# Performance work log

Hardware: AMD Instinct MI355X
Metric: run time of the kernel (lower is better)

Reference implementation:

```python
import jax, jax.numpy as jnp
import numpy as np

N_SPECIES = 119
N_RADIAL = 5
N_BASIS = 7
R_MIN = 0.5
R_MAX = 6.0
UNITS = (512, 512)
EMB_NORM = 1.0 / np.sqrt(N_BASIS)
N_ATOMS = 20000
N_PAIRS = 800000
N_FEAT = 360  # gaussian moments for n_radial=5, n_contr=8

# triangular index sets for symmetric contractions
_t2i, _t2j = np.tril_indices(N_RADIAL)  # 15 unique (r,s) pairs
_t3 = np.array([(i, j, k) for i in range(N_RADIAL) for j in range(i + 1) for k in range(j + 1)])
_t3i, _t3j, _t3k = _t3[:, 0], _t3[:, 1], _t3[:, 2]  # 35 unique (r,s,t) triples


def _forward(R, Z, neighbor, offsets, embeddings, W1, b1, W2, b2, W3, b3):
    n_atoms = R.shape[0]
    idx_i, idx_j = neighbor[0], neighbor[1]
    # --- distance computation (free space, init_box == 0) ---
    dr_vec = R[idx_j] - R[idx_i] + offsets                      # (P,3)
    dr = jnp.sqrt(jnp.sum(dr_vec * dr_vec, axis=-1))            # (P,)
    dn = dr_vec / (dr + 1e-5)[:, None]                          # unit vectors
    # --- gaussian radial basis + species-pair embedding + cosine cutoff ---
    shifts = jnp.linspace(R_MIN, R_MAX, N_BASIS)
    betta = N_BASIS ** 2 / R_MAX ** 2
    rad_norm = (2.0 * betta / np.pi) ** 0.75
    basis = rad_norm * jnp.exp(-betta * (dr[:, None] - shifts) ** 2)   # (P,B)
    cutoff = 0.5 * (jnp.cos(np.pi * dr / R_MAX) + 1.0) * (dr < R_MAX)
    emb = embeddings[Z[idx_j], Z[idx_i]]                               # (P,R,B)
    radial = EMB_NORM * jnp.einsum('prb,pb->pr', emb, basis) * cutoff[:, None]  # (P,R)
    # --- geometric moments, aggregated per central atom ---
    m1 = radial[:, :, None] * dn[:, None, :]                    # (P,R,3)
    m2 = m1[..., None] * dn[:, None, None, :]                   # (P,R,3,3)
    m3 = m2[..., None] * dn[:, None, None, None, :]             # (P,R,3,3,3)
    seg = lambda x: jax.ops.segment_sum(x, idx_i, num_segments=n_atoms)
    M0, M1, M2, M3 = seg(radial), seg(m1), seg(m2), seg(m3)
    # --- invariant contractions (gaussian moments) ---
    c1 = jnp.einsum('ari,asi->ars', M1, M1)[:, _t2i, _t2j]
    c2 = jnp.einsum('arij,asij->ars', M2, M2)[:, _t2i, _t2j]
    c3 = jnp.einsum('arijk,asijk->ars', M3, M3)[:, _t2i, _t2j]
    c4 = jnp.einsum('arij,asik,atjk->arst', M2, M2, M2)[:, _t3i, _t3j, _t3k]
    c5 = jnp.einsum('ari,asj,atij->arst', M1, M1, M2)[:, _t2i, _t2j].reshape(n_atoms, -1)
    c6 = jnp.einsum('arijk,asijl,atkl->arst', M3, M3, M2)[:, _t2i, _t2j].reshape(n_atoms, -1)
    c7 = jnp.einsum('arijk,asij,atk->arst', M3, M2, M1).reshape(n_atoms, -1)
    feats = jnp.concatenate([M0, c1, c2, c3, c4, c5, c6, c7], axis=-1)  # (A,360)
    # --- vmapped per-atom NTK readout MLP (swish) ---
    h = jax.nn.swish(feats @ W1 / np.sqrt(N_FEAT) + 0.1 * b1)
    h = jax.nn.swish(h @ W2 / np.sqrt(UNITS[0]) + 0.1 * b2)
    out = h @ W3 / np.sqrt(UNITS[1]) + 0.1 * b3                 # (A,1)
    # --- mask padded atoms (Z == 0) ---
    out = out * (Z > 0)[:, None]
    return out


def setup_inputs() -> dict:
    key = jax.random.key(0)
    ks = jax.random.split(key, 8)
    R = jax.random.uniform(ks[0], (N_ATOMS, 3), jnp.float32) * 12.0  # 12 A cube
    Z = jax.random.randint(ks[1], (N_ATOMS,), 0, N_SPECIES, jnp.int32)
    neighbor = jax.random.randint(ks[2], (2, N_PAIRS), 0, N_ATOMS, jnp.int32)
    # avoid degenerate self pairs (dr == 0 would NaN the unit vector grad)
    idx_i, idx_j = neighbor[0], neighbor[1]
    idx_j = jnp.where(idx_j == idx_i, (idx_j + 1) % N_ATOMS, idx_j)
    neighbor = jnp.stack([idx_i, idx_j], axis=0)
    box = jnp.zeros((3, 3), jnp.float32)
    offsets = jnp.zeros((N_PAIRS, 3), jnp.float32)
    embeddings = jax.random.normal(ks[3], (N_SPECIES, N_SPECIES, N_RADIAL, N_BASIS), jnp.float32)
    W1 = jax.random.normal(ks[4], (N_FEAT, UNITS[0]), jnp.float32)
    b1 = jnp.zeros((UNITS[0],), jnp.float32)
    W2 = jax.random.normal(ks[5], (UNITS[0], UNITS[1]), jnp.float32)
    b2 = jnp.zeros((UNITS[1],), jnp.float32)
    W3 = jax.random.normal(ks[6], (UNITS[1], 1), jnp.float32)
    b3 = jnp.zeros((1,), jnp.float32)
    return dict(R=R, Z=Z, neighbor=neighbor, box=box, offsets=offsets,
                embeddings=embeddings, W1=W1, b1=b1, W2=W2, b2=b2, W3=W3, b3=b3)


def reference(R, Z, neighbor, box, offsets, embeddings, W1, b1, W2, b2, W3, b3):
    # box is unused: init_box == 0 selects the free-space displacement fn
    return _forward(R, Z, neighbor, offsets, embeddings, W1, b1, W2, b2, W3, b3)
```

## Files before the change

### kernel.cpp

```cpp
#include <hip/hip_runtime.h>
#include <hip/hip_bf16.h>
#include <cmath>

#define NSP 119
#define UNITS 512
#define NFEAT 360
#define KP1 384
#define CAP 128

typedef __attribute__((ext_vector_type(8))) short short8;
typedef __attribute__((ext_vector_type(4))) float floatx4;

__device__ __host__ constexpr int s2c(int i, int j) {
    return (i > j) ? i*(i+1)/2 + j : j*(j+1)/2 + i;
}
__device__ __host__ constexpr int s3c(int x, int y, int z) {
    int A = x > y ? x : y; A = A > z ? A : z;
    int C = x < y ? x : y; C = C < z ? C : z;
    int B = x + y + z - A - C;
    return A*(A+1)*(A+2)/6 + B*(B+1)/2 + C;
}

struct BasisConsts {
    float f0k;
    float kg;
    float scale;
    float c[6];
};

__global__ __launch_bounds__(256) void prep_kernel(
    const float* __restrict__ W1, const float* __restrict__ W2,
    __hip_bfloat16* __restrict__ W1t, __hip_bfloat16* __restrict__ W2t,
    int* __restrict__ counts, float* __restrict__ outbuf,
    const int* __restrict__ Z, const float* __restrict__ b3, int natoms)
{
    int b = blockIdx.x;
    if (b < 448) {
        __shared__ float tile[32][33];
        const float* W; __hip_bfloat16* Wt; int K, Kp, ik, in;
        if (b < 192) { W = W1; Wt = W1t; K = NFEAT; Kp = KP1; ik = b % 12; in = b / 12; }
        else { int b2 = b - 192; W = W2; Wt = W2t; K = UNITS; Kp = UNITS; ik = b2 & 15; in = b2 >> 4; }
        int tx = threadIdx.x & 31, ty = threadIdx.x >> 5;
        int n = in * 32 + tx;
        #pragma unroll
        for (int pp = 0; pp < 4; ++pp) {
            int kk = ty + pp * 8;
            int k = ik * 32 + kk;
            tile[kk][tx] = (k < K) ? W[(size_t)k * UNITS + n] : 0.f;
        }
        __syncthreads();
        #pragma unroll
        for (int pp = 0; pp < 4; ++pp) {
            int nn = ty + pp * 8;
            Wt[(size_t)(in * 32 + nn) * Kp + ik * 32 + tx] = __float2bfloat16(tile[tx][nn]);
        }
    } else {
        int idx = (b - 448) * 256 + threadIdx.x;
        if (idx < natoms) {
            counts[idx] = 0;
            outbuf[idx] = (Z[idx] > 0) ? 0.1f * b3[0] : 0.f;
        }
    }
}

__global__ __launch_bounds__(256) void pair_compute_kernel(
    const float* __restrict__ R, const int* __restrict__ Z,
    const int* __restrict__ nbr, const float* __restrict__ offsets,
    const float* __restrict__ emb, int* __restrict__ counts,
    float* __restrict__ tmpRec, int npairs, BasisConsts bc)
{
    int p = blockIdx.x * 256 + threadIdx.x;
    if (p >= npairs) return;
    int i = nbr[p];
    int j = nbr[npairs + p];
    float dx = R[3*j]   - R[3*i]   + offsets[3*p];
    float dy = R[3*j+1] - R[3*i+1] + offsets[3*p+1];
    float dz = R[3*j+2] - R[3*i+2] + offsets[3*p+2];
    float dr2 = fmaf(dz, dz, fmaf(dy, dy, dx*dx));
    if (dr2 >= 36.0f) return;
    int pos = atomicAdd(&counts[i], 1);
    if (pos >= CAP) return;

    float dr  = sqrtf(dr2);
    float inv = 1.0f / (dr + 1e-5f);
    float d0  = dr - 0.5f;
    float basis[7];
    basis[0] = exp2f(bc.f0k * d0 * d0);
    float G  = exp2f(bc.kg * dr);
    float cur = basis[0];
    #pragma unroll
    for (int b = 0; b < 6; ++b) { cur *= G * bc.c[b]; basis[b+1] = cur; }
    float cut = 0.5f * (__cosf(dr * 0.52359877559829887f) + 1.0f);
    float s = bc.scale * cut;

    const float* e = emb + ((size_t)Z[j] * NSP + Z[i]) * 35;
    float ev[35];
    __builtin_memcpy(ev, e, 35 * sizeof(float));

    float rec[8];
    #pragma unroll
    for (int r = 0; r < 5; ++r) {
        float acc = 0.f;
        #pragma unroll
        for (int b = 0; b < 7; ++b) acc += ev[r*7+b] * basis[b];
        rec[r] = s * acc;
    }
    rec[5] = dx * inv; rec[6] = dy * inv; rec[7] = dz * inv;
    float4* out = (float4*)(tmpRec + ((size_t)i * CAP + pos) * 8);
    out[0] = make_float4(rec[0], rec[1], rec[2], rec[3]);
    out[1] = make_float4(rec[4], rec[5], rec[6], rec[7]);
}

#define SREC 28
__global__ __launch_bounds__(256) void moment_kernel(
    const float* __restrict__ tmpRec, const int* __restrict__ counts,
    float* __restrict__ momG, int natoms)
{
    int wv = threadIdx.x >> 6, lane = threadIdx.x & 63;
    int a = blockIdx.x * 4 + wv;
    __shared__ float stage[4][64][SREC];

    int cnt = 0;
    if (a < natoms) cnt = min(counts[a], CAP);

    int cr0, pk0;
    if (lane < 5)       { cr0 = lane;            pk0 = 0; }
    else if (lane < 20) { int c = lane - 5;      cr0 = c / 3;  pk0 = 1 + c % 3; }
    else if (lane < 50) { int c = lane - 20;     cr0 = c / 6;  pk0 = 4 + c % 6; }
    else                { int c = lane - 50;     cr0 = c / 10; pk0 = 10 + c % 10; }
    int cr1 = 0, pk1 = 0;
    if (lane < 36) { int c = 14 + lane; cr1 = c / 10; pk1 = 10 + c % 10; }

    float acc0 = 0.f, acc1 = 0.f;
    for (int base = 0; base < cnt; base += 64) {
        int m = min(64, cnt - base);
        if (lane < m) {
            const float4* pd = (const float4*)(tmpRec + ((size_t)a * CAP + base + lane) * 8);
            float4 u = pd[0], v = pd[1];
            float x = v.y, y = v.z, z = v.w;
            float s2_0 = x*x, s2_1 = y*x, s2_2 = y*y, s2_3 = z*x, s2_4 = z*y, s2_5 = z*z;
            float* st = stage[wv][lane];
            ((float4*)st)[0] = u;
            ((float4*)st)[1] = make_float4(v.x, 1.0f, x, y);
            ((float4*)st)[2] = make_float4(z, s2_0, s2_1, s2_2);
            ((float4*)st)[3] = make_float4(s2_3, s2_4, s2_5, s2_0*x);
            ((float4*)st)[4] = make_float4(s2_0*y, s2_2*x, s2_2*y, s2_0*z);
            ((float4*)st)[5] = make_float4(s2_1*z, s2_2*z, s2_5*x, s2_5*y);
            ((float4*)st)[6] = make_float4(s2_5*z, 0.f, 0.f, 0.f);
        }
        __builtin_amdgcn_wave_barrier();
        for (int q = 0; q < m; ++q) {
            const float* s = stage[wv][q];
            acc0 += s[cr0] * s[5 + pk0];
            acc1 += s[cr1] * s[5 + pk1];
        }
        __builtin_amdgcn_wave_barrier();
    }
    size_t base = (size_t)(a >> 6) * 6400 + (size_t)(a & 63);
    momG[base + (size_t)lane * 64] = acc0;
    if (lane < 36) momG[base + (size_t)(64 + lane) * 64] = acc1;
}

#define LROW 390
__global__ __launch_bounds__(256) void feat_kernel(
    const float* __restrict__ momG, __hip_bfloat16* __restrict__ feats)
{
    constexpr int cT2I[15] = {0,1,1,2,2,2,3,3,3,3,4,4,4,4,4};
    constexpr int cT2J[15] = {0,0,1,0,1,2,0,1,2,3,0,1,2,3,4};
    constexpr int cT3A[35] = {0, 1,1,1, 2,2,2,2,2,2, 3,3,3,3,3,3,3,3,3,3, 4,4,4,4,4,4,4,4,4,4,4,4,4,4,4};
    constexpr int cT3B[35] = {0, 0,1,1, 0,1,1,2,2,2, 0,1,1,2,2,2,3,3,3,3, 0,1,1,2,2,2,3,3,3,3,4,4,4,4,4};
    constexpr int cT3C[35] = {0, 0,0,1, 0,0,1,0,1,2, 0,0,1,0,1,2,0,1,2,3, 0,0,1,0,1,2,0,1,2,3,0,1,2,3,4};
    constexpr float cW2[6]  = {1.f,2.f,1.f,2.f,2.f,1.f};
    constexpr float cW3[10] = {1.f,3.f,3.f,1.f,3.f,6.f,3.f,3.f,3.f,1.f};

    __shared__ __hip_bfloat16 ldsF[64][LROW];
    int wv = threadIdx.x >> 6, lane = threadIdx.x & 63;
    const float* mg = momG + (size_t)blockIdx.x * 6400 + lane;

    #define LDM(e) mg[(e) * 64]
    #define STF(f, v) ldsF[lane][(f)] = __float2bfloat16(v)

    if (wv == 0) {
        float m3[50], m2[30];
        #pragma unroll
        for (int e = 0; e < 50; ++e) m3[e] = LDM(50 + e);
        #pragma unroll
        for (int e = 0; e < 30; ++e) m2[e] = LDM(20 + e);
        #pragma unroll
        for (int p = 0; p < 10; ++p) {
            int r = cT2I[p], s = cT2J[p];
            float B2v[9];
            #pragma unroll
            for (int z = 0; z < 3; ++z)
                #pragma unroll
                for (int w = 0; w < 3; ++w) {
                    float acc = 0.f;
                    #pragma unroll
                    for (int x = 0; x < 3; ++x)
                        #pragma unroll
                        for (int y = 0; y < 3; ++y)
                            acc += m3[r*10 + s3c(x,y,z)] * m3[s*10 + s3c(x,y,w)];
                    B2v[z*3+w] = acc;
                }
            #pragma unroll
            for (int t = 0; t < 5; ++t) {
                float acc = 0.f;
                #pragma unroll
                for (int z = 0; z < 3; ++z)
                    #pragma unroll
                    for (int w = 0; w < 3; ++w)
                        acc += B2v[z*3+w] * m2[t*6 + s2c(z,w)];
                STF(160 + p*5 + t, acc);
            }
        }
    } else if (wv == 1) {
        float m0[5], m1[15], m2[30];
        #pragma unroll
        for (int e = 0; e < 5; ++e)  m0[e] = LDM(e);
        #pragma unroll
        for (int e = 0; e < 15; ++e) m1[e] = LDM(5 + e);
        #pragma unroll
        for (int e = 0; e < 30; ++e) m2[e] = LDM(20 + e);
        #pragma unroll
        for (int r = 0; r < 5; ++r) STF(r, m0[r]);
        #pragma unroll
        for (int p = 0; p < 15; ++p) {
            int r = cT2I[p], s = cT2J[p];
            float v1 = m1[r*3]*m1[s*3] + m1[r*3+1]*m1[s*3+1] + m1[r*3+2]*m1[s*3+2];
            STF(5 + p, v1);
            float v2 = 0.f;
            #pragma unroll
            for (int k = 0; k < 6; ++k) v2 += cW2[k] * m2[r*6+k] * m2[s*6+k];
            STF(20 + p, v2);
        }
        #pragma unroll
        for (int q = 0; q < 35; ++q) {
            int r = cT3A[q], s = cT3B[q], t = cT3C[q];
            float v = 0.f;
            #pragma unroll
            for (int x = 0; x < 3; ++x)
                #pragma unroll
                for (int y = 0; y < 3; ++y) {
                    float d = 0.f;
                    #pragma unroll
                    for (int z = 0; z < 3; ++z)
                        d += m2[s*6 + s2c(x,z)] * m2[t*6 + s2c(y,z)];
                    v += m2[r*6 + s2c(x,y)] * d;
                }
            STF(50 + q, v);
        }
        #pragma unroll
        for (int f = NFEAT; f < KP1; ++f) STF(f, 0.f);
    } else if (wv == 2) {
        float m1[15], m2[30], m3[50];
        #pragma unroll
        for (int e = 0; e < 15; ++e) m1[e] = LDM(5 + e);
        #pragma unroll
        for (int e = 0; e < 30; ++e) m2[e] = LDM(20 + e);
        #pragma unroll
        for (int e = 0; e < 50; ++e) m3[e] = LDM(50 + e);
        #pragma unroll
        for (int p = 10; p < 15; ++p) {
            int r = cT2I[p], s = cT2J[p];
            float B2v[9];
            #pragma unroll
            for (int z = 0; z < 3; ++z)
                #pragma unroll
                for (int w = 0; w < 3; ++w) {
                    float acc = 0.f;
                    #pragma unroll
                    for (int x = 0; x < 3; ++x)
                        #pragma unroll
                        for (int y = 0; y < 3; ++y)
                            acc += m3[r*10 + s3c(x,y,z)] * m3[s*10 + s3c(x,y,w)];
                    B2v[z*3+w] = acc;
                }
            #pragma unroll
            for (int t = 0; t < 5; ++t) {
                float acc = 0.f;
                #pragma unroll
                for (int z = 0; z < 3; ++z)
                    #pragma unroll
                    for (int w = 0; w < 3; ++w)
                        acc += B2v[z*3+w] * m2[t*6 + s2c(z,w)];
                STF(160 + p*5 + t, acc);
            }
        }
        #pragma unroll
        for (int p = 0; p < 15; ++p) {
            int r = cT2I[p], s = cT2J[p];
            float o[9];
            #pragma unroll
            for (int x = 0; x < 3; ++x)
                #pragma unroll
                for (int y = 0; y < 3; ++y) o[x*3+y] = m1[r*3+x] * m1[s*3+y];
            #pragma unroll
            for (int t = 0; t < 5; ++t) {
                float v = 0.f;
                #pragma unroll
                for (int x = 0; x < 3; ++x)
                    #pragma unroll
                    for (int y = 0; y < 3; ++y)
                        v += o[x*3+y] * m2[t*6 + s2c(x,y)];
                STF(85 + p*5 + t, v);
            }
        }
    } else {
        float m1[15], m2[30], m3[50];
        #pragma unroll
        for (int e = 0; e < 15; ++e) m1[e] = LDM(5 + e);
        #pragma unroll
        for (int e = 0; e < 30; ++e) m2[e] = LDM(20 + e);
        #pragma unroll
        for (int e = 0; e < 50; ++e) m3[e] = LDM(50 + e);
        #pragma unroll
        for (int p = 0; p < 15; ++p) {
            int r = cT2I[p], s = cT2J[p];
            float v = 0.f;
            #pragma unroll
            for (int k = 0; k < 10; ++k) v += cW3[k] * m3[r*10+k] * m3[s*10+k];
            STF(35 + p, v);
        }
        #pragma unroll
        for (int r = 0; r < 5; ++r)
            #pragma unroll
            for (int s = 0; s < 5; ++s) {
                float A3z[3];
                #pragma unroll
                for (int z = 0; z < 3; ++z) {
                    float v = 0.f;
                    #pragma unroll
                    for (int x = 0; x < 3; ++x)
                        #pragma unroll
                        for (int y = 0; y < 3; ++y)
                            v += m3[r*10 + s3c(x,y,z)] * m2[s*6 + s2c(x,y)];
                    A3z[z] = v;
                }
                #pragma unroll
                for (int t = 0; t < 5; ++t) {
                    float v = A3z[0]*m1[t*3] + A3z[1]*m1[t*3+1] + A3z[2]*m1[t*3+2];
                    STF(235 + r*25 + s*5 + t, v);
                }
            }
    }
    __syncthreads();

    __hip_bfloat16* dst = feats + (size_t)blockIdx.x * 64 * KP1;
    #pragma unroll
    for (int rr = 0; rr < 16; ++rr) {
        int row = wv * 16 + rr;
        #pragma unroll
        for (int it = 0; it < 3; ++it) {
            uint32_t v = *(const uint32_t*)&ldsF[row][(it*64 + lane)*2];
            *(uint32_t*)&dst[(size_t)row * KP1 + (size_t)(it*64 + lane)*2] = v;
        }
    }
    #undef LDM
    #undef STF
}

__global__ __launch_bounds__(256) void gemm_mfma_swish(
    const __hip_bfloat16* __restrict__ A, const __hip_bfloat16* __restrict__ Bt,
    const float* __restrict__ bias, __hip_bfloat16* __restrict__ C,
    const float* __restrict__ w3, float* __restrict__ outacc,
    const int* __restrict__ Zmask,
    int Kp, int M, int Mtiles, float alpha, float a3, int fuse)
{
    __shared__ float4 As[2][512];
    __shared__ float4 Bs[2][512];
    int tid = threadIdx.x;
    int wave = tid >> 6, lane = tid & 63;
    int quad = lane >> 4, l16 = lane & 15;
    int wm = wave >> 1, wn = wave & 1;
    int bid = blockIdx.x;
    int mt = (bid >> 5) * 8 + (bid & 7);
    int nt = (bid >> 3) & 3;
    if (mt >= Mtiles) return;
    int rowBase = mt * 128;
    int colBase = nt * 128;

    floatx4 acc[4][4] = {};

    int rA0 = tid >> 2, cA = tid & 3;
    int rA1 = rA0 + 64;
    int pA0 = rA0 * 4 + (cA ^ ((rA0 >> 1) & 3));
    int pA1 = rA1 * 4 + (cA ^ ((rA1 >> 1) & 3));

    const char* pa0 = (const char*)(A  + (size_t)(rowBase + rA0) * Kp + cA * 8);
    const char* pa1 = (const char*)(A  + (size_t)(rowBase + rA1) * Kp + cA * 8);
    const char* pb0 = (const char*)(Bt + (size_t)(colBase + rA0) * Kp + cA * 8);
    const char* pb1 = (const char*)(Bt + (size_t)(colBase + rA1) * Kp + cA * 8);

    int posA[4], posB[4];
    #pragma unroll
    for (int t = 0; t < 4; ++t) {
        int rr = wm * 64 + t * 16 + l16;
        posA[t] = rr * 4 + (quad ^ ((rr >> 1) & 3));
    }
    #pragma unroll
    for (int u = 0; u < 4; ++u) {
        int cc = wn * 64 + u * 16 + l16;
        posB[u] = cc * 4 + (quad ^ ((cc >> 1) & 3));
    }

    int nK = Kp >> 5;
    float4 ra0 = *(const float4*)pa0;
    float4 ra1 = *(const float4*)pa1;
    float4 rb0 = *(const float4*)pb0;
    float4 rb1 = *(const float4*)pb1;

    for (int kt = 0; kt < nK; ++kt) {
        int buf = kt & 1;
        As[buf][pA0] = ra0;
        As[buf][pA1] = ra1;
        Bs[buf][pA0] = rb0;
        Bs[buf][pA1] = rb1;
        __syncthreads();
        if (kt + 1 < nK) {
            int off = (kt + 1) << 6;
            ra0 = *(const float4*)(pa0 + off);
            ra1 = *(const float4*)(pa1 + off);
            rb0 = *(const float4*)(pb0 + off);
            rb1 = *(const float4*)(pb1 + off);
        }
        short8 af[4], bf[4];
        #pragma unroll
        for (int t = 0; t < 4; ++t) af[t] = *(const short8*)(As[buf] + posA[t]);
        #pragma unroll
        for (int u = 0; u < 4; ++u) bf[u] = *(const short8*)(Bs[buf] + posB[u]);
        #pragma unroll
        for (int t = 0; t < 4; ++t)
            #pragma unroll
            for (int u = 0; u < 4; ++u)
                acc[t][u] = __builtin_amdgcn_mfma_f32_16x16x32_bf16(
                    af[t], bf[u], acc[t][u], 0, 0, 0);
    }

    if (!fuse) {
        #pragma unroll
        for (int u = 0; u < 4; ++u) {
            int col = colBase + wn * 64 + u * 16 + l16;
            float bc = 0.1f * bias[col];
            #pragma unroll
            for (int t = 0; t < 4; ++t) {
                int row0 = rowBase + wm * 64 + t * 16 + quad * 4;
                #pragma unroll
                for (int r = 0; r < 4; ++r) {
                    float x = alpha * acc[t][u][r] + bc;
                    float v = x / (1.f + expf(-x));
                    C[(size_t)(row0 + r) * UNITS + col] = __float2bfloat16(v);
                }
            }
        }
    } else {
        float rowsum[4][4] = {};
        #pragma unroll
        for (int u = 0; u < 4; ++u) {
            int col = colBase + wn * 64 + u * 16 + l16;
            float bc = 0.1f * bias[col];
            float w3c = w3[col] * a3;
            #pragma unroll
            for (int t = 0; t < 4; ++t)
                #pragma unroll
                for (int r = 0; r < 4; ++r) {
                    float x = alpha * acc[t][u][r] + bc;
                    float v = x / (1.f + expf(-x));
                    rowsum[t][r] += v * w3c;
                }
        }
        #pragma unroll
        for (int t = 0; t < 4; ++t)
            #pragma unroll
            for (int r = 0; r < 4; ++r) {
                float s = rowsum[t][r];
                s += __shfl_xor(s, 1, 64);
                s += __shfl_xor(s, 2, 64);
                s += __shfl_xor(s, 4, 64);
                s += __shfl_xor(s, 8, 64);
                rowsum[t][r] = s;
            }
        if (l16 == 0) {
            #pragma unroll
            for (int t = 0; t < 4; ++t) {
                int row0 = rowBase + wm * 64 + t * 16 + quad * 4;
                #pragma unroll
                for (int r = 0; r < 4; ++r) {
                    int row = row0 + r;
                    if (row < M && Zmask[row] > 0)
                        atomicAdd(&outacc[row], rowsum[t][r]);
                }
            }
        }
    }
}

static inline size_t align_up(size_t x, size_t a) { return (x + a - 1) & ~(a - 1); }

extern "C" void kernel_launch(void* const* d_in, const int* in_sizes, int n_in,
                              void* d_out, int out_size, void* d_ws, size_t ws_size,
                              hipStream_t stream)
{
    const float* R       = (const float*)d_in[0];
    const int*   Z       = (const int*)  d_in[1];
    const int*   nbr     = (const int*)  d_in[2];
    const float* offsets = (const float*)d_in[4];
    const float* emb     = (const float*)d_in[5];
    const float* W1      = (const float*)d_in[6];
    const float* b1      = (const float*)d_in[7];
    const float* W2      = (const float*)d_in[8];
    const float* b2      = (const float*)d_in[9];
    const float* W3      = (const float*)d_in[10];
    const float* b3      = (const float*)d_in[11];

    int natoms = in_sizes[0] / 3;
    int npairs = in_sizes[2] / 2;
    int Mpad = ((natoms + 127) / 128) * 128;
    int Mtiles = Mpad / 128;

    char* ws = (char*)d_ws;
    size_t off = 0;
    int* counts = (int*)(ws + off); off = align_up(off + natoms*4, 256);
    float* tmpRec = (float*)(ws + off); off = align_up(off + (size_t)natoms*CAP*8*4, 256);
    float* momG = (float*)(ws + off); off = align_up(off + (size_t)Mpad*100*4, 256);
    __hip_bfloat16* W1t   = (__hip_bfloat16*)(ws + off); off = align_up(off + (size_t)UNITS*KP1*2, 256);
    __hip_bfloat16* W2t   = (__hip_bfloat16*)(ws + off); off = align_up(off + (size_t)UNITS*UNITS*2, 256);
    __hip_bfloat16* feats = (__hip_bfloat16*)(ws + off); off = align_up(off + (size_t)Mpad*KP1*2, 256);
    __hip_bfloat16* h1    = (__hip_bfloat16*)(ws + off); off = align_up(off + (size_t)Mpad*UNITS*2, 256);

    BasisConsts bc;
    {
        const double betta = 49.0 / 36.0;
        const double delta = 5.5 / 6.0;
        const double log2e = 1.4426950408889634073599246810;
        bc.f0k = (float)(-betta * log2e);
        bc.kg  = (float)(2.0 * betta * delta * log2e);
        for (int b = 0; b < 6; ++b)
            bc.c[b] = (float)exp(-betta * delta * (1.0 + delta * (2*b + 1)));
        bc.scale = (float)(pow(2.0 * betta / M_PI, 0.75) / sqrt(7.0));
    }

    int prepBlocks = 448 + (natoms + 255) / 256;
    prep_kernel<<<dim3(prepBlocks), 256, 0, stream>>>(
        W1, W2, W1t, W2t, counts, (float*)d_out, Z, b3, natoms);

    int pgrid = (npairs + 255) / 256;
    pair_compute_kernel<<<dim3(pgrid), 256, 0, stream>>>(
        R, Z, nbr, offsets, emb, counts, tmpRec, npairs, bc);

    moment_kernel<<<dim3(Mpad / 4), 256, 0, stream>>>(
        tmpRec, counts, momG, natoms);
    feat_kernel<<<dim3(Mpad / 64), 256, 0, stream>>>(momG, feats);

    float a1 = 1.0f / sqrtf((float)NFEAT);
    float a2 = 1.0f / sqrtf((float)UNITS);
    int gemmGrid = ((Mtiles + 7) / 8) * 8 * 4;
    gemm_mfma_swish<<<dim3(gemmGrid), 256, 0, stream>>>(
        feats, W1t, b1, h1, nullptr, nullptr, nullptr, KP1, natoms, Mtiles, a1, 0.f, 0);
    gemm_mfma_swish<<<dim3(gemmGrid), 256, 0, stream>>>(
        h1, W2t, b2, nullptr, W3, (float*)d_out, Z, UNITS, natoms, Mtiles, a2, a2, 1);
}
```

Measured before the change: 201.1 us.

## Merge weight prep into pair kernel and load GEMM tiles directly into LDS

The weight transpose and output init now run as extra blocks of the pair-compute kernel, and the counts buffer is cleared with an async memset. This removes one separate launch and lets the prep work overlap with the pair work. The GEMM now uses global_load_lds to copy A/B tiles straight into double-buffered LDS with a swizzled source address, instead of staging them through registers. That frees registers and cuts instruction overhead, but it relies on the LDS layout matching the wave-ordered direct-load layout and moves the barrier to the end of each iteration.

```diff
diff --git a/kernel.cpp b/kernel.cpp
--- a/kernel.cpp
+++ b/kernel.cpp
@@ -10,6 +10,13 @@
 
 typedef __attribute__((ext_vector_type(8))) short short8;
 typedef __attribute__((ext_vector_type(4))) float floatx4;
+
+#define AS1 __attribute__((address_space(1)))
+#define AS3 __attribute__((address_space(3)))
+
+__device__ __forceinline__ void gload_lds16(const void* g, void* l) {
+    __builtin_amdgcn_global_load_lds((AS1 void*)(size_t)g, (AS3 void*)l, 16, 0, 0);
+}
 
 __device__ __host__ constexpr int s2c(int i, int j) {
     return (i > j) ? i*(i+1)/2 + j : j*(j+1)/2 + i;
@@ -28,48 +35,47 @@
     float c[6];
 };
 
-__global__ __launch_bounds__(256) void prep_kernel(
-    const float* __restrict__ W1, const float* __restrict__ W2,
-    __hip_bfloat16* __restrict__ W1t, __hip_bfloat16* __restrict__ W2t,
-    int* __restrict__ counts, float* __restrict__ outbuf,
-    const int* __restrict__ Z, const float* __restrict__ b3, int natoms)
-{
-    int b = blockIdx.x;
-    if (b < 448) {
-        __shared__ float tile[32][33];
-        const float* W; __hip_bfloat16* Wt; int K, Kp, ik, in;
-        if (b < 192) { W = W1; Wt = W1t; K = NFEAT; Kp = KP1; ik = b % 12; in = b / 12; }
-        else { int b2 = b - 192; W = W2; Wt = W2t; K = UNITS; Kp = UNITS; ik = b2 & 15; in = b2 >> 4; }
-        int tx = threadIdx.x & 31, ty = threadIdx.x >> 5;
-        int n = in * 32 + tx;
-        #pragma unroll
-        for (int pp = 0; pp < 4; ++pp) {
-            int kk = ty + pp * 8;
-            int k = ik * 32 + kk;
-            tile[kk][tx] = (k < K) ? W[(size_t)k * UNITS + n] : 0.f;
-        }
-        __syncthreads();
-        #pragma unroll
-        for (int pp = 0; pp < 4; ++pp) {
-            int nn = ty + pp * 8;
-            Wt[(size_t)(in * 32 + nn) * Kp + ik * 32 + tx] = __float2bfloat16(tile[tx][nn]);
-        }
-    } else {
-        int idx = (b - 448) * 256 + threadIdx.x;
-        if (idx < natoms) {
-            counts[idx] = 0;
-            outbuf[idx] = (Z[idx] > 0) ? 0.1f * b3[0] : 0.f;
-        }
-    }
-}
-
-__global__ __launch_bounds__(256) void pair_compute_kernel(
+__global__ __launch_bounds__(256) void pair_prep_kernel(
     const float* __restrict__ R, const int* __restrict__ Z,
     const int* __restrict__ nbr, const float* __restrict__ offsets,
     const float* __restrict__ emb, int* __restrict__ counts,
-    float* __restrict__ tmpRec, int npairs, BasisConsts bc)
+    float* __restrict__ tmpRec, int npairs, BasisConsts bc,
+    const float* __restrict__ W1, const float* __restrict__ W2,
+    __hip_bfloat16* __restrict__ W1t, __hip_bfloat16* __restrict__ W2t,
+    float* __restrict__ outbuf, const float* __restrict__ b3,
+    int pgrid, int natoms)
 {
-    int p = blockIdx.x * 256 + threadIdx.x;
+    int blk = blockIdx.x;
+    if (blk >= pgrid) {
+        int b = blk - pgrid;
+        if (b < 448) {
+            __shared__ float tile[32][33];
+            const float* W; __hip_bfloat16* Wt; int K, Kp, ik, in;
+            if (b < 192) { W = W1; Wt = W1t; K = NFEAT; Kp = KP1; ik = b % 12; in = b / 12; }
+            else { int b2 = b - 192; W = W2; Wt = W2t; K = UNITS; Kp = UNITS; ik = b2 & 15; in = b2 >> 4; }
+            int tx = threadIdx.x & 31, ty = threadIdx.x >> 5;
+            int n = in * 32 + tx;
+            #pragma unroll
+            for (int pp = 0; pp < 4; ++pp) {
+                int kk = ty + pp * 8;
+                int k = ik * 32 + kk;
+                tile[kk][tx] = (k < K) ? W[(size_t)k * UNITS + n] : 0.f;
+            }
+            __syncthreads();
+            #pragma unroll
+            for (int pp = 0; pp < 4; ++pp) {
+                int nn = ty + pp * 8;
+                Wt[(size_t)(in * 32 + nn) * Kp + ik * 32 + tx] = __float2bfloat16(tile[tx][nn]);
+            }
+        } else {
+            int idx = (b - 448) * 256 + threadIdx.x;
+            if (idx < natoms)
+                outbuf[idx] = (Z[idx] > 0) ? 0.1f * b3[0] : 0.f;
+        }
+        return;
+    }
+
+    int p = blk * 256 + threadIdx.x;
     if (p >= npairs) return;
     int i = nbr[p];
     int j = nbr[npairs + p];
@@ -381,15 +387,17 @@
 
     floatx4 acc[4][4] = {};
 
-    int rA0 = tid >> 2, cA = tid & 3;
-    int rA1 = rA0 + 64;
-    int pA0 = rA0 * 4 + (cA ^ ((rA0 >> 1) & 3));
-    int pA1 = rA1 * 4 + (cA ^ ((rA1 >> 1) & 3));
-
-    const char* pa0 = (const char*)(A  + (size_t)(rowBase + rA0) * Kp + cA * 8);
-    const char* pa1 = (const char*)(A  + (size_t)(rowBase + rA1) * Kp + cA * 8);
-    const char* pb0 = (const char*)(Bt + (size_t)(colBase + rA0) * Kp + cA * 8);
-    const char* pb1 = (const char*)(Bt + (size_t)(colBase + rA1) * Kp + cA * 8);
+    int r0 = tid >> 2, c0 = (tid & 3) ^ ((r0 >> 1) & 3);
+    int r1 = r0 + 64,  c1 = (tid & 3) ^ ((r1 >> 1) & 3);
+
+    const char* gA0 = (const char*)A  + ((size_t)(rowBase + r0) * Kp) * 2 + c0 * 16;
+    const char* gA1 = (const char*)A  + ((size_t)(rowBase + r1) * Kp) * 2 + c1 * 16;
+    const char* gB0 = (const char*)Bt + ((size_t)(colBase + r0) * Kp) * 2 + c0 * 16;
+    const char* gB1 = (const char*)Bt + ((size_t)(colBase + r1) * Kp) * 2 + c1 * 16;
+
+    char* lA = (char*)As;
+    char* lB = (char*)Bs;
+    int wvoff = wave << 10;
 
     int posA[4], posB[4];
     #pragma unroll
@@ -404,24 +412,25 @@
     }
 
     int nK = Kp >> 5;
-    float4 ra0 = *(const float4*)pa0;
-    float4 ra1 = *(const float4*)pa1;
-    float4 rb0 = *(const float4*)pb0;
-    float4 rb1 = *(const float4*)pb1;
+
+    {
+        int lo = wvoff;
+        gload_lds16(gA0, lA + lo);
+        gload_lds16(gA1, lA + lo + 4096);
+        gload_lds16(gB0, lB + lo);
+        gload_lds16(gB1, lB + lo + 4096);
+    }
+    __syncthreads();
 
     for (int kt = 0; kt < nK; ++kt) {
         int buf = kt & 1;
-        As[buf][pA0] = ra0;
-        As[buf][pA1] = ra1;
-        Bs[buf][pA0] = rb0;
-        Bs[buf][pA1] = rb1;
-        __syncthreads();
         if (kt + 1 < nK) {
-            int off = (kt + 1) << 6;
-            ra0 = *(const float4*)(pa0 + off);
-            ra1 = *(const float4*)(pa1 + off);
-            rb0 = *(const float4*)(pb0 + off);
-            rb1 = *(const float4*)(pb1 + off);
+            int go = (kt + 1) << 6;
+            int lo = ((buf ^ 1) << 13) + wvoff;
+            gload_lds16(gA0 + go, lA + lo);
+            gload_lds16(gA1 + go, lA + lo + 4096);
+            gload_lds16(gB0 + go, lB + lo);
+            gload_lds16(gB1 + go, lB + lo + 4096);
         }
         short8 af[4], bf[4];
         #pragma unroll
@@ -434,6 +443,7 @@
             for (int u = 0; u < 4; ++u)
                 acc[t][u] = __builtin_amdgcn_mfma_f32_16x16x32_bf16(
                     af[t], bf[u], acc[t][u], 0, 0, 0);
+        __syncthreads();
     }
 
     if (!fuse) {
@@ -539,13 +549,13 @@
         bc.scale = (float)(pow(2.0 * betta / M_PI, 0.75) / sqrt(7.0));
     }
 
-    int prepBlocks = 448 + (natoms + 255) / 256;
-    prep_kernel<<<dim3(prepBlocks), 256, 0, stream>>>(
-        W1, W2, W1t, W2t, counts, (float*)d_out, Z, b3, natoms);
+    hipMemsetAsync(counts, 0, (size_t)natoms * sizeof(int), stream);
 
     int pgrid = (npairs + 255) / 256;
-    pair_compute_kernel<<<dim3(pgrid), 256, 0, stream>>>(
-        R, Z, nbr, offsets, emb, counts, tmpRec, npairs, bc);
+    int totalBlocks = pgrid + 448 + (natoms + 255) / 256;
+    pair_prep_kernel<<<dim3(totalBlocks), 256, 0, stream>>>(
+        R, Z, nbr, offsets, emb, counts, tmpRec, npairs, bc,
+        W1, W2, W1t, W2t, (float*)d_out, b3, pgrid, natoms);
 
     moment_kernel<<<dim3(Mpad / 4), 256, 0, stream>>>(
         tmpRec, counts, momG, natoms);
```

After: 200.4 us. Within noise of the previous version (-0.3%).
